# Kernel tuning notes

Hardware: AMD Instinct MI355X
Metric: run time of the kernel (lower is better)

Reference implementation:

```python
import jax, jax.numpy as jnp
import numpy as np


def setup_inputs() -> dict:
    key = jax.random.key(0)
    ks = jax.random.split(key, 4)
    B, S, D, V = 2, 2048, 768, 50257
    scale = 1.0 / np.sqrt(D)
    x = jax.random.normal(ks[0], (B, S, D), dtype=jnp.float32)
    W_vocab = jax.random.normal(ks[1], (V, D), dtype=jnp.float32) * scale
    b_vocab = jnp.zeros((V,), dtype=jnp.float32)
    W_lin = jax.random.normal(ks[2], (D, D), dtype=jnp.float32) * scale
    b_lin = jnp.zeros((D,), dtype=jnp.float32)
    return {"x": x, "W_vocab": W_vocab, "b_vocab": b_vocab, "W_lin": W_lin, "b_lin": b_lin}


def reference(x, W_vocab, b_vocab, W_lin, b_lin):
    # vocab_attention_layer(x): [B,S,D] @ [D,V] + b -> [B,S,V]
    logits = jnp.einsum('bsd,vd->bsv', x, W_vocab) + b_vocab
    va = jax.nn.softmax(logits, axis=-1)                      # [B,S,V]
    # einsum('bij,jk->bik', va, weight): contract vocab against embedding rows
    va_weight = jnp.einsum('bsv,vd->bsd', va, W_vocab)        # [B,S,D]
    # final nn.Linear(d_model, d_model): y = h @ W^T + b
    return jnp.einsum('bsd,ed->bse', va_weight, W_lin) + b_lin
```

## Files before the change

### kernel.cpp

```cpp
#include <hip/hip_runtime.h>
#include <hip/hip_bf16.h>
#include <stdint.h>

typedef float f32x4 __attribute__((ext_vector_type(4)));
typedef short s16x8 __attribute__((ext_vector_type(8)));
typedef unsigned short u16;

#define M_ROWS 4096
#define DIM    768
#define VOCAB  50257
#define VP2    50432
#define KTOT   788

#define OFF_XB     0ull
#define OFF_WLB    6291456ull
#define OFF_WVB    7471104ull
#define OFF_WVT    84934656ull
#define OFF_P      162398208ull
#define OFF_ORUN   229507072ull
#define OFF_LROW   242089984ull
#define OFF_BROW   242106368ull
#define OFF_KEYS   242122752ull
#define OFF_H      242122880ull

__device__ __forceinline__ u16 f2bf(float f) {
    union { float f; unsigned u; } x; x.f = f;
    return (u16)((x.u + 0x7fffu + ((x.u >> 16) & 1u)) >> 16);
}
__device__ __forceinline__ float bf2f_hi(unsigned u) {
    union { unsigned u; float f; } x; x.u = u & 0xffff0000u; return x.f;
}
__device__ __forceinline__ float bf2f_lo(unsigned u) {
    union { unsigned u; float f; } x; x.u = u << 16; return x.f;
}
__device__ __forceinline__ unsigned fkey(float f) {
    union { float f; unsigned u; } x; x.f = f;
    return (x.u & 0x80000000u) ? ~x.u : (x.u | 0x80000000u);
}
__device__ __forceinline__ float fkey_dec(unsigned k) {
    union { unsigned u; float f; } x;
    x.u = (k & 0x80000000u) ? (k & 0x7fffffffu) : ~k;
    return x.f;
}
__device__ __forceinline__ void glds16(const u16* g, u16* l) {
    __builtin_amdgcn_global_load_lds(
        (const __attribute__((address_space(1))) unsigned int*)g,
        (__attribute__((address_space(3))) unsigned int*)l,
        16, 0, 0);
}

__global__ __launch_bounds__(256) void cast_bf16(const float* __restrict__ src,
                                                 u16* __restrict__ dst, int n4) {
    int i = blockIdx.x * 256 + threadIdx.x;
    if (i >= n4) return;
    float4 v = ((const float4*)src)[i];
    ushort4 o;
    o.x = f2bf(v.x); o.y = f2bf(v.y); o.z = f2bf(v.z); o.w = f2bf(v.w);
    ((ushort4*)dst)[i] = o;
}

__global__ __launch_bounds__(256) void prep_wvb(const float* __restrict__ wv,
                                                u16* __restrict__ wvb, int ntask) {
    int t = blockIdx.x * 256 + threadIdx.x;
    if (t >= ntask) return;
    int v = t / 96, ch = t % 96;
    uint4 pk = {0u, 0u, 0u, 0u};
    if (v < VOCAB) {
        const float* p = wv + (size_t)v * DIM + ch * 8;
        float4 f0 = ((const float4*)p)[0];
        float4 f1 = ((const float4*)p)[1];
        pk.x = (unsigned)f2bf(f0.x) | ((unsigned)f2bf(f0.y) << 16);
        pk.y = (unsigned)f2bf(f0.z) | ((unsigned)f2bf(f0.w) << 16);
        pk.z = (unsigned)f2bf(f1.x) | ((unsigned)f2bf(f1.y) << 16);
        pk.w = (unsigned)f2bf(f1.z) | ((unsigned)f2bf(f1.w) << 16);
    }
    *(uint4*)(wvb + (size_t)v * DIM + ch * 8) = pk;
}

__global__ void init_keys(unsigned* keys) {
    keys[0] = 0u;
    keys[1] = fkey(-3.0e38f);
}

__global__ __launch_bounds__(256) void wnorm(const u16* __restrict__ wvb,
                                             unsigned* __restrict__ keys) {
    __shared__ float part[128];
    int tid = threadIdx.x;
    int vb = blockIdx.x * 32;
    int vl = tid & 31, cg = tid >> 5;
    float s = 0.f;
    #pragma unroll
    for (int it = 0; it < 12; ++it) {
        int ch = cg + 8 * it;
        uint4 pk = *(const uint4*)(wvb + (size_t)(vb + vl) * DIM + ch * 8);
        const unsigned* pw = (const unsigned*)&pk;
        #pragma unroll
        for (int k = 0; k < 4; ++k) {
            float lo = bf2f_lo(pw[k]), hi = bf2f_hi(pw[k]);
            s += lo * lo + hi * hi;
        }
    }
    s += __shfl_xor(s, 32);
    int w = tid >> 6, lane = tid & 63;
    if (lane < 32) part[w * 32 + lane] = s;
    __syncthreads();
    if (tid < 32) {
        float t = part[tid] + part[32 + tid] + part[64 + tid] + part[96 + tid];
        float n = sqrtf(t);
        #pragma unroll
        for (int msk = 1; msk < 32; msk <<= 1) n = fmaxf(n, __shfl_xor(n, msk));
        if (tid == 0) atomicMax(&keys[0], __float_as_uint(n));
    }
}

__global__ __launch_bounds__(256) void bmax_k(const float* __restrict__ bv,
                                              unsigned* __restrict__ keys) {
    int i = blockIdx.x * 256 + threadIdx.x;
    float v = (i < VOCAB) ? bv[i] : -3.0e38f;
    #pragma unroll
    for (int msk = 1; msk < 64; msk <<= 1) v = fmaxf(v, __shfl_xor(v, msk));
    if ((threadIdx.x & 63) == 0) atomicMax(&keys[1], fkey(v));
}

__global__ __launch_bounds__(256) void xnorm(const float* __restrict__ x,
                                             const unsigned* __restrict__ keys,
                                             float* __restrict__ Brow) {
    int w = threadIdx.x >> 6, lane = threadIdx.x & 63;
    int r = blockIdx.x * 4 + w;
    const float4* p = (const float4*)(x + (size_t)r * DIM);
    float s = 0.f;
    #pragma unroll
    for (int it = 0; it < 3; ++it) {
        float4 v = p[it * 64 + lane];
        s += v.x * v.x + v.y * v.y + v.z * v.z + v.w * v.w;
    }
    #pragma unroll
    for (int msk = 1; msk < 64; msk <<= 1) s += __shfl_xor(s, msk);
    if (lane == 0) {
        float Wn = __uint_as_float(keys[0]);
        float bm = fkey_dec(keys[1]);
        Brow[r] = sqrtf(s) * Wn * 1.01f + bm + 0.1f;
    }
}

__global__ __launch_bounds__(256) void prep_wvtb(const u16* __restrict__ wvb,
                                                 u16* __restrict__ wvtb) {
    __shared__ u16 tile[32][776];
    int vb = blockIdx.x * 32;
    int kt = vb >> 6;
    int vhalf = (vb >> 5) & 1;
    int tid = threadIdx.x;
    #pragma unroll
    for (int it = 0; it < 12; ++it) {
        int task = tid + 256 * it;
        int row = task / 96, ch = task % 96;
        *(uint4*)(&tile[row][ch * 8]) = *(const uint4*)(wvb + (size_t)(vb + row) * DIM + ch * 8);
    }
    __syncthreads();
    #pragma unroll
    for (int it = 0; it < 12; ++it) {
        int task = tid + 256 * it;
        int nt = task >> 10, rem = task & 1023;
        int dd = rem >> 2, vg = rem & 3;
        u16 t8[8];
        #pragma unroll
        for (int j = 0; j < 8; ++j) t8[j] = tile[vg * 8 + j][nt * 256 + dd];
        uint4 pk;
        pk.x = (unsigned)t8[0] | ((unsigned)t8[1] << 16);
        pk.y = (unsigned)t8[2] | ((unsigned)t8[3] << 16);
        pk.z = (unsigned)t8[4] | ((unsigned)t8[5] << 16);
        pk.w = (unsigned)t8[6] | ((unsigned)t8[7] << 16);
        *(uint4*)(wvtb + (size_t)(nt * KTOT + kt) * 16384 + dd * 64 + vhalf * 32 + vg * 8) = pk;
    }
}


template<int MH, int NH>
__device__ __forceinline__ void mfma_quad(f32x4 (&acc)[8][4],
                                          const s16x8 (&afr)[4][2],
                                          const s16x8 (&bfr)[2][2][2]) {
    #pragma unroll
    for (int mi = 0; mi < 4; ++mi)
        #pragma unroll
        for (int ni = 0; ni < 2; ++ni) {
            f32x4 a_ = acc[MH * 4 + mi][NH * 2 + ni];
            a_ = __builtin_amdgcn_mfma_f32_16x16x32_bf16(afr[mi][0], bfr[NH][ni][0], a_, 0, 0, 0);
            a_ = __builtin_amdgcn_mfma_f32_16x16x32_bf16(afr[mi][1], bfr[NH][ni][1], a_, 0, 0, 0);
            acc[MH * 4 + mi][NH * 2 + ni] = a_;
        }
}

#define STG(g, pitch, rowbase, kcol, ldst) do {                                   \
    const u16* _s0 = (g) + (size_t)((rowbase) + rlo) * (pitch) + (kcol) + offu;   \
    const u16* _s1 = _s0 + (size_t)64 * (pitch);                                  \
    glds16(_s0, (u16*)(ldst) + (size_t)tid * 8);                                  \
    glds16(_s1, (u16*)(ldst) + (size_t)tid * 8 + 4096);                           \
} while (0)

#define RD_A(buf, mh) do { _Pragma("unroll")                                              \
    for (int _mi = 0; _mi < 4; ++_mi) {                                                   \
        afr[_mi][0] = *(const s16x8*)((buf) + ((abase + ((mh)*4 + _mi)*2048)      ^ asw));\
        afr[_mi][1] = *(const s16x8*)((buf) + ((abase + ((mh)*4 + _mi)*2048 + 64) ^ asw));\
    } } while (0)

#define RD_B(buf, nh) do { _Pragma("unroll")                                              \
    for (int _ni = 0; _ni < 2; ++_ni) {                                                   \
        bfr[nh][_ni][0] = *(const s16x8*)((buf) + ((bbase + ((nh)*2 + _ni)*2048)      ^ asw));\
        bfr[nh][_ni][1] = *(const s16x8*)((buf) + ((bbase + ((nh)*2 + _ni)*2048 + 64) ^ asw));\
    } } while (0)

#define SP1() __builtin_amdgcn_s_setprio(1)
#define SP0() __builtin_amdgcn_s_setprio(0)
#define BARRIER() __builtin_amdgcn_s_barrier()
#define WAIT_VM4() do { asm volatile("s_waitcnt vmcnt(4)" ::: "memory"); \
    __builtin_amdgcn_sched_barrier(0); } while (0)
#define WAIT_LGKM0() do { asm volatile("s_waitcnt lgkmcnt(0)" ::: "memory"); \
    __builtin_amdgcn_sched_barrier(0); } while (0)

__device__ __forceinline__ void kloop256(char* LDS,
                                         const u16* __restrict__ gA, int pA,
                                         const u16* __restrict__ gB, int pB, int ksB,
                                         int NT, int tid, f32x4 (&acc)[8][4]) {
    const int lane = tid & 63, w = tid >> 6;
    const int c = lane & 15, q = (lane >> 4) & 3;
    const int wm = w & 1, wn = w >> 1;
    const int asw = (c & 7) << 4;
    const int abase = wm * 16384 + c * 128 + q * 16;
    const int bbase = (wn >> 1) * 16384 + (wn & 1) * 8192 + c * 128 + q * 16;
    const int rlo = tid >> 3;
    const int offu = ((tid & 7) * 8) ^ ((rlo & 7) << 3);
    char* A0 = LDS;
    char* B0 = LDS + 32768;
    char* A1 = LDS + 65536;
    char* B1 = LDS + 98304;
    s16x8 afr[4][2], bfr[2][2][2];
    const int ktN = NT - 1;

    STG(gA, pA, 0,   0, A0);
    STG(gA, pA, 128, 0, A0 + 16384);
    STG(gB, pB, 0,   0, B0);
    STG(gB, pB, 128, 0, B0 + 16384);
    {
        int t1 = (1 <= ktN) ? 1 : ktN;
        STG(gB, pB, 0,   t1 * ksB, B1);
        STG(gB, pB, 128, t1 * ksB, B1 + 16384);
    }
    WAIT_VM4();
    BARRIER();

    const int nit = NT >> 1;
    #pragma unroll 1
    for (int it2 = 0; it2 < nit; ++it2) {
        int t1 = (2 * it2 + 1 <= ktN) ? 2 * it2 + 1 : ktN;
        int t2 = (2 * it2 + 2 <= ktN) ? 2 * it2 + 2 : ktN;
        int t3 = (2 * it2 + 3 <= ktN) ? 2 * it2 + 3 : ktN;
        RD_A(A0, 0); RD_B(B0, 0); RD_B(B0, 1);
        STG(gA, pA, 0,   t1 * 64, A1);
        STG(gA, pA, 128, t1 * 64, A1 + 16384);
        SP1(); mfma_quad<0, 0>(acc, afr, bfr); SP0();
        WAIT_LGKM0();
        BARRIER();
        STG(gB, pB, 0,   t2 * ksB, B0);
        STG(gB, pB, 128, t2 * ksB, B0 + 16384);
        SP1(); mfma_quad<0, 1>(acc, afr, bfr); SP0();
        RD_A(A0, 1);
        SP1(); mfma_quad<1, 0>(acc, afr, bfr);
               mfma_quad<1, 1>(acc, afr, bfr); SP0();
        WAIT_VM4();
        BARRIER();
        RD_A(A1, 0); RD_B(B1, 0); RD_B(B1, 1);
        STG(gA, pA, 0,   t2 * 64, A0);
        STG(gA, pA, 128, t2 * 64, A0 + 16384);
        SP1(); mfma_quad<0, 0>(acc, afr, bfr); SP0();
        WAIT_LGKM0();
        BARRIER();
        STG(gB, pB, 0,   t3 * ksB, B1);
        STG(gB, pB, 128, t3 * ksB, B1 + 16384);
        SP1(); mfma_quad<0, 1>(acc, afr, bfr); SP0();
        RD_A(A1, 1);
        SP1(); mfma_quad<1, 0>(acc, afr, bfr);
               mfma_quad<1, 1>(acc, afr, bfr); SP0();
        WAIT_VM4();
        BARRIER();
    }
}

__global__ __launch_bounds__(512, 2) void gemm1(
    const u16* __restrict__ xb, const u16* __restrict__ wvb,
    const float* __restrict__ bvocab, const float* __restrict__ Brow,
    u16* __restrict__ P, float* __restrict__ Lrow, int v0, int CN) {
    __shared__ __align__(16) char LDS[131072];
    __shared__ float BL[256];
    int tid = threadIdx.x;
    int nwg = gridDim.x, cpx = nwg >> 3;
    int bid = blockIdx.x;
    bid = (bid & 7) * cpx + (bid >> 3);
    int mt = bid & 15, nt = bid >> 4;
    if (tid < 256) BL[tid] = Brow[mt * 256 + tid];
    f32x4 acc[8][4];
    #pragma unroll
    for (int i = 0; i < 8; ++i)
        #pragma unroll
        for (int j = 0; j < 4; ++j) acc[i][j] = (f32x4){0.f, 0.f, 0.f, 0.f};
    kloop256(LDS, xb + (size_t)(mt * 256) * DIM, DIM,
             wvb + (size_t)(v0 + nt * 256) * DIM, DIM, 64, 12, tid, acc);

    int lane = tid & 63, w = tid >> 6, c = lane & 15, q = (lane >> 4) & 3;
    int wm = w & 1, wn = w >> 1;
    float bvv[4]; bool vok[4];
    #pragma unroll
    for (int n = 0; n < 4; ++n) {
        int vg = v0 + nt * 256 + wn * 64 + n * 16 + c;
        vok[n] = vg < VOCAB;
        bvv[n] = vok[n] ? bvocab[vg] : 0.f;
    }
    #pragma unroll
    for (int m = 0; m < 8; ++m)
        #pragma unroll
        for (int jr = 0; jr < 4; ++jr) {
            int rloc = wm * 128 + m * 16 + q * 4 + jr;
            float B = BL[rloc];
            float s = 0.f;
            #pragma unroll
            for (int n = 0; n < 4; ++n) {
                float z = acc[m][n][jr] + bvv[n];
                float e = vok[n] ? __expf(z - B) : 0.f;
                acc[m][n][jr] = e;
                s += e;
            }
            s += __shfl_xor(s, 1); s += __shfl_xor(s, 2);
            s += __shfl_xor(s, 4); s += __shfl_xor(s, 8);
            if (c == 0) atomicAdd(&Lrow[mt * 256 + rloc], s);
        }
    u16* Pt = (u16*)LDS;
    #pragma unroll
    for (int h = 0; h < 2; ++h) {
        if (h) __syncthreads();
        if (wm == h) {
            #pragma unroll
            for (int m = 0; m < 8; ++m)
                #pragma unroll
                for (int jr = 0; jr < 4; ++jr) {
                    int r = m * 16 + q * 4 + jr;
                    #pragma unroll
                    for (int n = 0; n < 4; ++n)
                        Pt[r * 256 + wn * 64 + n * 16 + c] = f2bf(acc[m][n][jr]);
                }
        }
        __syncthreads();
        #pragma unroll
        for (int itc = 0; itc < 8; ++itc) {
            int task = tid + itc * 512;
            int r = task >> 5, chn = task & 31;
            uint4 pk = *(const uint4*)(Pt + r * 256 + chn * 8);
            *(uint4*)(P + (size_t)(mt * 256 + h * 128 + r) * CN + nt * 256 + chn * 8) = pk;
        }
    }
}

__global__ __launch_bounds__(512, 2) void gemm2(
    const u16* __restrict__ P, const u16* __restrict__ wvtb,
    float* __restrict__ Orun, int CN, int v0, int KT) {
    __shared__ __align__(16) char LDS[131072];
    int tid = threadIdx.x;
    int nwg = gridDim.x, cpx = nwg >> 3;
    int bid = blockIdx.x;
    bid = (bid & 7) * cpx + (bid >> 3);
    int mt = bid & 15;
    int rest = bid >> 4;
    int nt = rest % 3, s = rest / 3;
    int ks0 = ((KT + 9) / 10) * 2;
    int k0 = s * ks0;
    if (k0 >= KT) return;
    int NTs = (k0 + ks0 <= KT) ? ks0 : (KT - k0);
    f32x4 acc[8][4];
    #pragma unroll
    for (int i = 0; i < 8; ++i)
        #pragma unroll
        for (int j = 0; j < 4; ++j) acc[i][j] = (f32x4){0.f, 0.f, 0.f, 0.f};
    kloop256(LDS, P + (size_t)(mt * 256) * CN + k0 * 64, CN,
             wvtb + (size_t)(nt * KTOT + (v0 >> 6) + k0) * 16384, 64, 16384,
             NTs, tid, acc);

    int lane = tid & 63, w = tid >> 6, c = lane & 15, q = (lane >> 4) & 3;
    int wm = w & 1, wn = w >> 1;
    #pragma unroll
    for (int m = 0; m < 8; ++m)
        #pragma unroll
        for (int n = 0; n < 4; ++n) {
            int col = nt * 256 + wn * 64 + n * 16 + c;
            #pragma unroll
            for (int jr = 0; jr < 4; ++jr) {
                int row = mt * 256 + wm * 128 + m * 16 + q * 4 + jr;
                atomicAdd(&Orun[(size_t)row * DIM + col], acc[m][n][jr]);
            }
        }
}

__global__ __launch_bounds__(256) void final_h(const float* __restrict__ Orun,
                                               const float* __restrict__ Lrow,
                                               u16* __restrict__ h) {
    int idx = blockIdx.x * 256 + threadIdx.x;
    if (idx >= M_ROWS * DIM) return;
    int r = idx / DIM;
    h[idx] = f2bf(Orun[idx] / Lrow[r]);
}

__global__ __launch_bounds__(256, 2) void final_gemm(const u16* __restrict__ h,
                                                     const u16* __restrict__ wlb,
                                                     const float* __restrict__ blin,
                                                     float* __restrict__ out) {
    __shared__ u16 At[4096];
    __shared__ u16 Bt[4096];
    int mb = blockIdx.x & 31, eb = blockIdx.x >> 5;
    int tid = threadIdx.x;
    int w = tid >> 6, lane = tid & 63, q = lane >> 4, c = lane & 15;
    int wm = w & 1, wn = w >> 1;
    int trow = tid >> 2, tch = tid & 3;
    const u16* gA0 = h + (size_t)(mb * 128 + trow) * DIM + tch * 8;
    const u16* gA1 = h + (size_t)(mb * 128 + 64 + trow) * DIM + tch * 8;
    const u16* gB0 = wlb + (size_t)(eb * 128 + trow) * DIM + tch * 8;
    const u16* gB1 = wlb + (size_t)(eb * 128 + 64 + trow) * DIM + tch * 8;
    f32x4 acc[4][4];
    #pragma unroll
    for (int i = 0; i < 4; ++i)
        #pragma unroll
        for (int j = 0; j < 4; ++j) acc[i][j] = (f32x4){0.f, 0.f, 0.f, 0.f};

    for (int ko = 0; ko < 24; ++ko) {
        glds16(gA0 + ko * 32, At + tid * 8);
        glds16(gA1 + ko * 32, At + (tid + 256) * 8);
        glds16(gB0 + ko * 32, Bt + tid * 8);
        glds16(gB1 + ko * 32, Bt + (tid + 256) * 8);
        __syncthreads();
        s16x8 af[4], bf[4];
        #pragma unroll
        for (int i = 0; i < 4; ++i)
            af[i] = *(const s16x8*)(At + (wm * 64 + i * 16 + c) * 32 + q * 8);
        #pragma unroll
        for (int j = 0; j < 4; ++j)
            bf[j] = *(const s16x8*)(Bt + (wn * 64 + j * 16 + c) * 32 + q * 8);
        #pragma unroll
        for (int i = 0; i < 4; ++i)
            #pragma unroll
            for (int j = 0; j < 4; ++j)
                acc[i][j] = __builtin_amdgcn_mfma_f32_16x16x32_bf16(af[i], bf[j], acc[i][j], 0, 0, 0);
        __syncthreads();
    }
    #pragma unroll
    for (int j = 0; j < 4; ++j) {
        int e = eb * 128 + wn * 64 + j * 16 + c;
        float bl = blin[e];
        #pragma unroll
        for (int i = 0; i < 4; ++i) {
            #pragma unroll
            for (int jr = 0; jr < 4; ++jr) {
                int row = mb * 128 + wm * 64 + i * 16 + q * 4 + jr;
                out[(size_t)row * DIM + e] = acc[i][j][jr] + bl;
            }
        }
    }
}

extern "C" void kernel_launch(void* const* d_in, const int* in_sizes, int n_in,
                              void* d_out, int out_size, void* d_ws, size_t ws_size,
                              hipStream_t stream) {
    const float* x  = (const float*)d_in[0];
    const float* Wv = (const float*)d_in[1];
    const float* bv = (const float*)d_in[2];
    const float* Wl = (const float*)d_in[3];
    const float* bl = (const float*)d_in[4];
    float* out = (float*)d_out;
    char* ws = (char*)d_ws;

    u16* xb   = (u16*)(ws + OFF_XB);
    u16* wlb  = (u16*)(ws + OFF_WLB);
    u16* wvb  = (u16*)(ws + OFF_WVB);
    u16* wvtb = (u16*)(ws + OFF_WVT);
    u16* P    = (u16*)(ws + OFF_P);
    float* Orun  = (float*)(ws + OFF_ORUN);
    float* Lrow  = (float*)(ws + OFF_LROW);
    float* Brow  = (float*)(ws + OFF_BROW);
    unsigned* keys = (unsigned*)(ws + OFF_KEYS);
    u16* h       = (u16*)(ws + OFF_H);

    cast_bf16<<<(M_ROWS * DIM / 4 + 255) / 256, 256, 0, stream>>>(x, xb, M_ROWS * DIM / 4);
    cast_bf16<<<(DIM * DIM / 4 + 255) / 256, 256, 0, stream>>>(Wl, wlb, DIM * DIM / 4);
    {
        int ntask = VP2 * 96;
        prep_wvb<<<(ntask + 255) / 256, 256, 0, stream>>>(Wv, wvb, ntask);
    }
    init_keys<<<1, 1, 0, stream>>>(keys);
    hipMemsetAsync(Orun, 0, (size_t)M_ROWS * DIM * 4, stream);
    hipMemsetAsync(Lrow, 0, (size_t)M_ROWS * 4, stream);
    wnorm<<<VP2 / 32, 256, 0, stream>>>(wvb, keys);
    bmax_k<<<(VOCAB + 255) / 256, 256, 0, stream>>>(bv, keys);
    xnorm<<<M_ROWS / 4, 256, 0, stream>>>(x, keys, Brow);
    prep_wvtb<<<VP2 / 32, 256, 0, stream>>>(wvb, wvtb);

    static const int chunk_start[7] = {0, 32, 64, 96, 128, 160, 192};
    static const int chunk_cnt[7]   = {32, 32, 32, 32, 32, 32, 5};
    for (int ci = 0; ci < 7; ++ci) {
        int cnt = chunk_cnt[ci];
        int v0 = chunk_start[ci] * 256;
        int CN = cnt * 256;
        int KT = CN / 64;
        gemm1<<<16 * cnt, 512, 0, stream>>>(xb, wvb, bv, Brow, P, Lrow, v0, CN);
        gemm2<<<240, 512, 0, stream>>>(P, wvtb, Orun, CN, v0, KT);
    }
    final_h<<<(M_ROWS * DIM + 255) / 256, 256, 0, stream>>>(Orun, Lrow, h);
    final_gemm<<<192, 256, 0, stream>>>(h, wlb, bl, out);
}
```

Measured before the change: 1.363 ms.

## Rewrite second GEMM with full-width 64x768 tiles and 32-deep K-slab layout

Replaces the 256x256-tile split-K gemm2 with a kernel where each workgroup owns 64 rows across all 768 output columns. It streams W_vocab^T in 32-vocab K slabs, stored in a new transposed layout, and the P tiles in 64-wide K chunks, double buffered with direct global-to-LDS loads. Each block reads P once instead of three times, and the grid becomes 64 row tiles by 4 K splits. The trade-off is smaller K steps with more barriers per unit of work, and still fp32 atomics into the running output.

```diff
diff --git a/kernel.cpp b/kernel.cpp
--- a/kernel.cpp
+++ b/kernel.cpp
@@ -10,7 +10,7 @@
 #define DIM    768
 #define VOCAB  50257
 #define VP2    50432
-#define KTOT   788
+#define KT32   1576
 
 #define OFF_XB     0ull
 #define OFF_WLB    6291456ull
@@ -143,12 +143,11 @@
     }
 }
 
-__global__ __launch_bounds__(256) void prep_wvtb(const u16* __restrict__ wvb,
-                                                 u16* __restrict__ wvtb) {
+__global__ __launch_bounds__(256) void prep_wvt32(const u16* __restrict__ wvb,
+                                                  u16* __restrict__ wvt32) {
     __shared__ u16 tile[32][776];
-    int vb = blockIdx.x * 32;
-    int kt = vb >> 6;
-    int vhalf = (vb >> 5) & 1;
+    int kt = blockIdx.x;
+    int vb = kt * 32;
     int tid = threadIdx.x;
     #pragma unroll
     for (int it = 0; it < 12; ++it) {
@@ -160,20 +159,18 @@
     #pragma unroll
     for (int it = 0; it < 12; ++it) {
         int task = tid + 256 * it;
-        int nt = task >> 10, rem = task & 1023;
-        int dd = rem >> 2, vg = rem & 3;
+        int d = task >> 2, vg = task & 3;
         u16 t8[8];
         #pragma unroll
-        for (int j = 0; j < 8; ++j) t8[j] = tile[vg * 8 + j][nt * 256 + dd];
+        for (int j = 0; j < 8; ++j) t8[j] = tile[vg * 8 + j][d];
         uint4 pk;
         pk.x = (unsigned)t8[0] | ((unsigned)t8[1] << 16);
         pk.y = (unsigned)t8[2] | ((unsigned)t8[3] << 16);
         pk.z = (unsigned)t8[4] | ((unsigned)t8[5] << 16);
         pk.w = (unsigned)t8[6] | ((unsigned)t8[7] << 16);
-        *(uint4*)(wvtb + (size_t)(nt * KTOT + kt) * 16384 + dd * 64 + vhalf * 32 + vg * 8) = pk;
-    }
-}
-
+        *(uint4*)(wvt32 + (size_t)kt * 24576 + d * 32 + vg * 8) = pk;
+    }
+}
 
 template<int MH, int NH>
 __device__ __forceinline__ void mfma_quad(f32x4 (&acc)[8][4],
@@ -358,41 +355,94 @@
     }
 }
 
-__global__ __launch_bounds__(512, 2) void gemm2(
-    const u16* __restrict__ P, const u16* __restrict__ wvtb,
-    float* __restrict__ Orun, int CN, int v0, int KT) {
-    __shared__ __align__(16) char LDS[131072];
+__global__ __launch_bounds__(512, 2) void gemm2v2(
+    const u16* __restrict__ P, const u16* __restrict__ wvt32,
+    float* __restrict__ Orun, int CN, int v0, int ksK) {
+    __shared__ __align__(16) char LDS[114688];
     int tid = threadIdx.x;
-    int nwg = gridDim.x, cpx = nwg >> 3;
-    int bid = blockIdx.x;
-    bid = (bid & 7) * cpx + (bid >> 3);
-    int mt = bid & 15;
-    int rest = bid >> 4;
-    int nt = rest % 3, s = rest / 3;
-    int ks0 = ((KT + 9) / 10) * 2;
-    int k0 = s * ks0;
-    if (k0 >= KT) return;
-    int NTs = (k0 + ks0 <= KT) ? ks0 : (KT - k0);
-    f32x4 acc[8][4];
-    #pragma unroll
-    for (int i = 0; i < 8; ++i)
-        #pragma unroll
-        for (int j = 0; j < 4; ++j) acc[i][j] = (f32x4){0.f, 0.f, 0.f, 0.f};
-    kloop256(LDS, P + (size_t)(mt * 256) * CN + k0 * 64, CN,
-             wvtb + (size_t)(nt * KTOT + (v0 >> 6) + k0) * 16384, 64, 16384,
-             NTs, tid, acc);
-
-    int lane = tid & 63, w = tid >> 6, c = lane & 15, q = (lane >> 4) & 3;
-    int wm = w & 1, wn = w >> 1;
-    #pragma unroll
-    for (int m = 0; m < 8; ++m)
-        #pragma unroll
-        for (int n = 0; n < 4; ++n) {
-            int col = nt * 256 + wn * 64 + n * 16 + c;
+    int bid = (blockIdx.x & 7) * 32 + (blockIdx.x >> 3);
+    int mt = bid & 63, s = bid >> 6;
+    int lane = tid & 63, w = tid >> 6;
+    int c = lane & 15, q = (lane >> 4) & 3;
+    char* B0p = LDS;
+    char* B1p = LDS + 49152;
+    char* A0p = LDS + 98304;
+    char* A1p = LDS + 106496;
+    int rloA = tid >> 3;
+    int offuA = (((tid & 7) ^ (rloA & 7)) * 8);
+    const u16* gA = P + (size_t)(mt * 64 + rloA) * CN + offuA;
+    int xa0 = (((0 * 4 + q) ^ (c & 7)) * 16);
+    int xa1 = (((1 * 4 + q) ^ (c & 7)) * 16);
+    int bku = ((q ^ (c & 3)) * 16);
+    int k32_0 = (v0 >> 5) + s * ksK * 2;
+    int kA0 = s * ksK;
+    int nss = ksK * 2;
+
+    f32x4 acc[4][6];
+    #pragma unroll
+    for (int i = 0; i < 4; ++i)
+        #pragma unroll
+        for (int j = 0; j < 6; ++j) acc[i][j] = (f32x4){0.f, 0.f, 0.f, 0.f};
+
+#define STGB(kt, buf) do { size_t _b = (size_t)(kt) * 24576;                    \
+    _Pragma("unroll") for (int _t = 0; _t < 6; ++_t) {                          \
+        int _lin = _t * 512 + tid; int _r = _lin >> 2, _ku = _lin & 3;          \
+        const u16* _src = wvt32 + _b + _r * 32 + ((_ku ^ (_r & 3)) * 8);        \
+        glds16(_src, (u16*)(buf) + (size_t)_lin * 8); } } while (0)
+#define STGA(k64, buf) glds16(gA + (size_t)(kA0 + (k64)) * 64, (u16*)(buf) + (size_t)tid * 8)
+
+    STGB(k32_0 + 0, B0p);
+    STGA(0, A0p);
+    STGB(k32_0 + ((nss > 1) ? 1 : 0), B1p);
+    asm volatile("s_waitcnt vmcnt(6)" ::: "memory");
+    __builtin_amdgcn_sched_barrier(0);
+    BARRIER();
+
+    s16x8 af[4], bf[6];
+    #pragma unroll 1
+    for (int ss = 0; ss < nss; ++ss) {
+        char* Bc = (ss & 1) ? B1p : B0p;
+        char* Ac = ((ss >> 1) & 1) ? A1p : A0p;
+        int xab = (ss & 1) ? xa1 : xa0;
+        #pragma unroll
+        for (int mi = 0; mi < 4; ++mi)
+            af[mi] = *(const s16x8*)(Ac + ((mi * 16 + c) * 128 + xab));
+        #pragma unroll
+        for (int j = 0; j < 6; ++j)
+            bf[j] = *(const s16x8*)(Bc + ((w * 96 + j * 16 + c) * 64 + bku));
+        SP1();
+        #pragma unroll
+        for (int mi = 0; mi < 4; ++mi)
+            #pragma unroll
+            for (int j = 0; j < 6; ++j)
+                acc[mi][j] = __builtin_amdgcn_mfma_f32_16x16x32_bf16(af[mi], bf[j], acc[mi][j], 0, 0, 0);
+        SP0();
+        WAIT_LGKM0();
+        BARRIER();
+        int s2 = (ss + 2 < nss) ? ss + 2 : nss - 1;
+        STGB(k32_0 + s2, Bc);
+        if ((ss & 1) == 0) {
+            int a2 = (ss >> 1) + 1; if (a2 > ksK - 1) a2 = ksK - 1;
+            STGA(a2, ((ss >> 1) & 1) ? A0p : A1p);
+            asm volatile("s_waitcnt vmcnt(7)" ::: "memory");
+        } else {
+            asm volatile("s_waitcnt vmcnt(6)" ::: "memory");
+        }
+        __builtin_amdgcn_sched_barrier(0);
+        BARRIER();
+    }
+#undef STGB
+#undef STGA
+
+    #pragma unroll
+    for (int mi = 0; mi < 4; ++mi)
+        #pragma unroll
+        for (int j = 0; j < 6; ++j) {
+            int col = w * 96 + j * 16 + c;
             #pragma unroll
             for (int jr = 0; jr < 4; ++jr) {
-                int row = mt * 256 + wm * 128 + m * 16 + q * 4 + jr;
-                atomicAdd(&Orun[(size_t)row * DIM + col], acc[m][n][jr]);
+                int row = mt * 64 + mi * 16 + q * 4 + jr;
+                atomicAdd(&Orun[(size_t)row * DIM + col], acc[mi][j][jr]);
             }
         }
 }
@@ -473,11 +523,11 @@
     float* out = (float*)d_out;
     char* ws = (char*)d_ws;
 
-    u16* xb   = (u16*)(ws + OFF_XB);
-    u16* wlb  = (u16*)(ws + OFF_WLB);
-    u16* wvb  = (u16*)(ws + OFF_WVB);
-    u16* wvtb = (u16*)(ws + OFF_WVT);
-    u16* P    = (u16*)(ws + OFF_P);
+    u16* xb    = (u16*)(ws + OFF_XB);
+    u16* wlb   = (u16*)(ws + OFF_WLB);
+    u16* wvb   = (u16*)(ws + OFF_WVB);
+    u16* wvt32 = (u16*)(ws + OFF_WVT);
+    u16* P     = (u16*)(ws + OFF_P);
     float* Orun  = (float*)(ws + OFF_ORUN);
     float* Lrow  = (float*)(ws + OFF_LROW);
     float* Brow  = (float*)(ws + OFF_BROW);
@@ -496,7 +546,7 @@
     wnorm<<<VP2 / 32, 256, 0, stream>>>(wvb, keys);
     bmax_k<<<(VOCAB + 255) / 256, 256, 0, stream>>>(bv, keys);
     xnorm<<<M_ROWS / 4, 256, 0, stream>>>(x, keys, Brow);
-    prep_wvtb<<<VP2 / 32, 256, 0, stream>>>(wvb, wvtb);
+    prep_wvt32<<<KT32, 256, 0, stream>>>(wvb, wvt32);
 
     static const int chunk_start[7] = {0, 32, 64, 96, 128, 160, 192};
     static const int chunk_cnt[7]   = {32, 32, 32, 32, 32, 32, 5};
@@ -504,9 +554,8 @@
         int cnt = chunk_cnt[ci];
         int v0 = chunk_start[ci] * 256;
         int CN = cnt * 256;
-        int KT = CN / 64;
         gemm1<<<16 * cnt, 512, 0, stream>>>(xb, wvb, bv, Brow, P, Lrow, v0, CN);
-        gemm2<<<240, 512, 0, stream>>>(P, wvtb, Orun, CN, v0, KT);
+        gemm2v2<<<256, 512, 0, stream>>>(P, wvt32, Orun, CN, v0, cnt);
     }
     final_h<<<(M_ROWS * DIM + 255) / 256, 256, 0, stream>>>(Orun, Lrow, h);
     final_gemm<<<192, 256, 0, stream>>>(h, wlb, bl, out);
```

New measurement: 1.438 ms. 1.06x slower.

## Rewrite gemm2 as 128x128 split-K tiles over a k32-blocked W layout

Applied to the files above, without the earlier changes.

Replaces the 256x256-tile, 512-thread pipelined gemm2 with a simple 128x128-tile, 256-thread kernel. It uses a new k32-blocked transposed vocab weight layout, a 4-way split-K and a 768-block grid. The vocab chunking also changes from 7 chunks of 32 to 5 chunks of 40, and the P buffer is enlarged to match. The goal is more parallelism and fewer launches. The cost is losing the double-buffered kloop256 pipeline, lower per-tile reuse, and more atomic traffic into Orun.

```diff
diff --git a/kernel.cpp b/kernel.cpp
--- a/kernel.cpp
+++ b/kernel.cpp
@@ -10,18 +10,18 @@
 #define DIM    768
 #define VOCAB  50257
 #define VP2    50432
-#define KTOT   788
+#define KT32   1576
 
 #define OFF_XB     0ull
 #define OFF_WLB    6291456ull
 #define OFF_WVB    7471104ull
 #define OFF_WVT    84934656ull
 #define OFF_P      162398208ull
-#define OFF_ORUN   229507072ull
-#define OFF_LROW   242089984ull
-#define OFF_BROW   242106368ull
-#define OFF_KEYS   242122752ull
-#define OFF_H      242122880ull
+#define OFF_ORUN   246284288ull
+#define OFF_LROW   258867200ull
+#define OFF_BROW   258883584ull
+#define OFF_KEYS   258899968ull
+#define OFF_H      258900096ull
 
 __device__ __forceinline__ u16 f2bf(float f) {
     union { float f; unsigned u; } x; x.f = f;
@@ -143,12 +143,11 @@
     }
 }
 
-__global__ __launch_bounds__(256) void prep_wvtb(const u16* __restrict__ wvb,
-                                                 u16* __restrict__ wvtb) {
+__global__ __launch_bounds__(256) void prep_wvt32(const u16* __restrict__ wvb,
+                                                  u16* __restrict__ wvt32) {
     __shared__ u16 tile[32][776];
-    int vb = blockIdx.x * 32;
-    int kt = vb >> 6;
-    int vhalf = (vb >> 5) & 1;
+    int kt = blockIdx.x;
+    int vb = kt * 32;
     int tid = threadIdx.x;
     #pragma unroll
     for (int it = 0; it < 12; ++it) {
@@ -160,20 +159,18 @@
     #pragma unroll
     for (int it = 0; it < 12; ++it) {
         int task = tid + 256 * it;
-        int nt = task >> 10, rem = task & 1023;
-        int dd = rem >> 2, vg = rem & 3;
+        int d = task >> 2, vg = task & 3;
         u16 t8[8];
         #pragma unroll
-        for (int j = 0; j < 8; ++j) t8[j] = tile[vg * 8 + j][nt * 256 + dd];
+        for (int j = 0; j < 8; ++j) t8[j] = tile[vg * 8 + j][d];
         uint4 pk;
         pk.x = (unsigned)t8[0] | ((unsigned)t8[1] << 16);
         pk.y = (unsigned)t8[2] | ((unsigned)t8[3] << 16);
         pk.z = (unsigned)t8[4] | ((unsigned)t8[5] << 16);
         pk.w = (unsigned)t8[6] | ((unsigned)t8[7] << 16);
-        *(uint4*)(wvtb + (size_t)(nt * KTOT + kt) * 16384 + dd * 64 + vhalf * 32 + vg * 8) = pk;
-    }
-}
-
+        *(uint4*)(wvt32 + (size_t)kt * 24576 + d * 32 + vg * 8) = pk;
+    }
+}
 
 template<int MH, int NH>
 __device__ __forceinline__ void mfma_quad(f32x4 (&acc)[8][4],
@@ -358,43 +355,63 @@
     }
 }
 
-__global__ __launch_bounds__(512, 2) void gemm2(
-    const u16* __restrict__ P, const u16* __restrict__ wvtb,
-    float* __restrict__ Orun, int CN, int v0, int KT) {
-    __shared__ __align__(16) char LDS[131072];
+__global__ __launch_bounds__(256, 2) void gemm2(
+    const u16* __restrict__ P, const u16* __restrict__ wvt32,
+    float* __restrict__ Orun, int CN, int v0, int kt32_total, int kts) {
+    __shared__ u16 At[4096];
+    __shared__ u16 Bt[4096];
+    int bid = blockIdx.x;
+    bid = (bid & 7) * 96 + (bid >> 3);
+    int mb = bid & 31;
+    int rest = bid >> 5;
+    int nb = rest % 6, s = rest / 6;
+    int kt0 = s * kts;
+    int kt1 = kt0 + kts; if (kt1 > kt32_total) kt1 = kt32_total;
     int tid = threadIdx.x;
-    int nwg = gridDim.x, cpx = nwg >> 3;
-    int bid = blockIdx.x;
-    bid = (bid & 7) * cpx + (bid >> 3);
-    int mt = bid & 15;
-    int rest = bid >> 4;
-    int nt = rest % 3, s = rest / 3;
-    int ks0 = ((KT + 9) / 10) * 2;
-    int k0 = s * ks0;
-    if (k0 >= KT) return;
-    int NTs = (k0 + ks0 <= KT) ? ks0 : (KT - k0);
-    f32x4 acc[8][4];
-    #pragma unroll
-    for (int i = 0; i < 8; ++i)
+    int w = tid >> 6, lane = tid & 63, q = lane >> 4, c = lane & 15;
+    int wm = w & 1, wn = w >> 1;
+    int trow = tid >> 2, tch = tid & 3;
+    const u16* gA0 = P + (size_t)(mb * 128 + trow) * CN + tch * 8;
+    const u16* gA1 = P + (size_t)(mb * 128 + 64 + trow) * CN + tch * 8;
+    const u16* wvtb = wvt32 + (size_t)(v0 >> 5) * 24576;
+    const u16* gB0 = wvtb + (size_t)(nb * 128 + trow) * 32 + tch * 8;
+    const u16* gB1 = wvtb + (size_t)(nb * 128 + 64 + trow) * 32 + tch * 8;
+    f32x4 acc[4][4];
+    #pragma unroll
+    for (int i = 0; i < 4; ++i)
         #pragma unroll
         for (int j = 0; j < 4; ++j) acc[i][j] = (f32x4){0.f, 0.f, 0.f, 0.f};
-    kloop256(LDS, P + (size_t)(mt * 256) * CN + k0 * 64, CN,
-             wvtb + (size_t)(nt * KTOT + (v0 >> 6) + k0) * 16384, 64, 16384,
-             NTs, tid, acc);
-
-    int lane = tid & 63, w = tid >> 6, c = lane & 15, q = (lane >> 4) & 3;
-    int wm = w & 1, wn = w >> 1;
-    #pragma unroll
-    for (int m = 0; m < 8; ++m)
-        #pragma unroll
-        for (int n = 0; n < 4; ++n) {
-            int col = nt * 256 + wn * 64 + n * 16 + c;
+
+    for (int kt = kt0; kt < kt1; ++kt) {
+        glds16(gA0 + kt * 32, At + tid * 8);
+        glds16(gA1 + kt * 32, At + (tid + 256) * 8);
+        glds16(gB0 + (size_t)kt * 24576, Bt + tid * 8);
+        glds16(gB1 + (size_t)kt * 24576, Bt + (tid + 256) * 8);
+        __syncthreads();
+        s16x8 af[4], bf[4];
+        #pragma unroll
+        for (int i = 0; i < 4; ++i)
+            af[i] = *(const s16x8*)(At + (wm * 64 + i * 16 + c) * 32 + q * 8);
+        #pragma unroll
+        for (int j = 0; j < 4; ++j)
+            bf[j] = *(const s16x8*)(Bt + (wn * 64 + j * 16 + c) * 32 + q * 8);
+        #pragma unroll
+        for (int i = 0; i < 4; ++i)
+            #pragma unroll
+            for (int j = 0; j < 4; ++j)
+                acc[i][j] = __builtin_amdgcn_mfma_f32_16x16x32_bf16(af[i], bf[j], acc[i][j], 0, 0, 0);
+        __syncthreads();
+    }
+    #pragma unroll
+    for (int i = 0; i < 4; ++i)
+        #pragma unroll
+        for (int j = 0; j < 4; ++j)
             #pragma unroll
             for (int jr = 0; jr < 4; ++jr) {
-                int row = mt * 256 + wm * 128 + m * 16 + q * 4 + jr;
-                atomicAdd(&Orun[(size_t)row * DIM + col], acc[m][n][jr]);
+                int row = mb * 128 + wm * 64 + i * 16 + q * 4 + jr;
+                int col = nb * 128 + wn * 64 + j * 16 + c;
+                atomicAdd(&Orun[(size_t)row * DIM + col], acc[i][j][jr]);
             }
-        }
 }
 
 __global__ __launch_bounds__(256) void final_h(const float* __restrict__ Orun,
@@ -473,11 +490,11 @@
     float* out = (float*)d_out;
     char* ws = (char*)d_ws;
 
-    u16* xb   = (u16*)(ws + OFF_XB);
-    u16* wlb  = (u16*)(ws + OFF_WLB);
-    u16* wvb  = (u16*)(ws + OFF_WVB);
-    u16* wvtb = (u16*)(ws + OFF_WVT);
-    u16* P    = (u16*)(ws + OFF_P);
+    u16* xb    = (u16*)(ws + OFF_XB);
+    u16* wlb   = (u16*)(ws + OFF_WLB);
+    u16* wvb   = (u16*)(ws + OFF_WVB);
+    u16* wvt32 = (u16*)(ws + OFF_WVT);
+    u16* P     = (u16*)(ws + OFF_P);
     float* Orun  = (float*)(ws + OFF_ORUN);
     float* Lrow  = (float*)(ws + OFF_LROW);
     float* Brow  = (float*)(ws + OFF_BROW);
@@ -496,17 +513,18 @@
     wnorm<<<VP2 / 32, 256, 0, stream>>>(wvb, keys);
     bmax_k<<<(VOCAB + 255) / 256, 256, 0, stream>>>(bv, keys);
     xnorm<<<M_ROWS / 4, 256, 0, stream>>>(x, keys, Brow);
-    prep_wvtb<<<VP2 / 32, 256, 0, stream>>>(wvb, wvtb);
-
-    static const int chunk_start[7] = {0, 32, 64, 96, 128, 160, 192};
-    static const int chunk_cnt[7]   = {32, 32, 32, 32, 32, 32, 5};
-    for (int ci = 0; ci < 7; ++ci) {
+    prep_wvt32<<<KT32, 256, 0, stream>>>(wvb, wvt32);
+
+    static const int chunk_start[5] = {0, 40, 80, 120, 160};
+    static const int chunk_cnt[5]   = {40, 40, 40, 40, 37};
+    for (int ci = 0; ci < 5; ++ci) {
         int cnt = chunk_cnt[ci];
         int v0 = chunk_start[ci] * 256;
         int CN = cnt * 256;
-        int KT = CN / 64;
+        int kt32 = CN / 32;
+        int kts = (kt32 + 3) / 4;
         gemm1<<<16 * cnt, 512, 0, stream>>>(xb, wvb, bv, Brow, P, Lrow, v0, CN);
-        gemm2<<<240, 512, 0, stream>>>(P, wvtb, Orun, CN, v0, KT);
+        gemm2<<<768, 256, 0, stream>>>(P, wvt32, Orun, CN, v0, kt32, kts);
     }
     final_h<<<(M_ROWS * DIM + 255) / 256, 256, 0, stream>>>(Orun, Lrow, h);
     final_gemm<<<192, 256, 0, stream>>>(h, wlb, bl, out);
```

After: 1.363 ms. About the same (-0.1%).
